# Optimization experiments

Hardware: AMD Instinct MI355X
Metric: run time of the kernel (lower is better)

## Reference

```python
import jax, jax.numpy as jnp
import numpy as np
import math

B, S, STATE, H, D = 4, 2048, 1024, 16, 64
N_ROT = 32  # int(0.5*64), even
ROPE_BASE = 10000.0


def setup_inputs() -> dict:
    key = jax.random.key(0)
    ks = jax.random.split(key, 8)
    q_src = jax.random.normal(ks[0], (B, S, STATE), jnp.float32)
    k_src = jax.random.normal(ks[1], (B, S, STATE), jnp.float32)
    v_src = jax.random.normal(ks[2], (B, S, STATE), jnp.float32)
    # causal position mask: True = masked (torch masked_fill semantics)
    position_mask = jnp.triu(jnp.ones((S, S), jnp.bool_), k=1)
    sd = 0.02
    Wq = jax.random.normal(ks[3], (H * D, STATE), jnp.float32) * sd
    Wk = jax.random.normal(ks[4], (H * D, STATE), jnp.float32) * sd
    Wv = jax.random.normal(ks[5], (H * D, STATE), jnp.float32) * sd
    Wo = jax.random.normal(ks[6], (STATE, H * D), jnp.float32) * sd
    return {"q_src": q_src, "k_src": k_src, "v_src": v_src,
            "position_mask": position_mask,
            "Wq": Wq, "Wk": Wk, "Wv": Wv, "Wo": Wo}


def _rotate_half(x):
    x1, x2 = jnp.split(x, 2, axis=-1)
    return jnp.concatenate([-x2, x1], axis=-1)


def _rope(q, k, offset):
    # q,k: [B,H,S,N_ROT]; positions: k at arange(Sk), q at offset+arange(Sq)
    inv_freq = 1.0 / (ROPE_BASE ** (jnp.arange(0, N_ROT, 2, dtype=jnp.float32) / N_ROT))
    def sincos(pos):
        freqs = pos[:, None] * inv_freq[None, :]          # [S, N_ROT/2]
        emb = jnp.concatenate([freqs, freqs], axis=-1)    # [S, N_ROT]
        return jnp.sin(emb), jnp.cos(emb)
    sk, ck = sincos(jnp.arange(k.shape[-2], dtype=jnp.float32))
    sq, cq = sincos(offset + jnp.arange(q.shape[-2], dtype=jnp.float32))
    q = q * cq + _rotate_half(q) * sq
    k = k * ck + _rotate_half(k) * sk
    return q, k


def reference(q_src, k_src, v_src, position_mask, Wq, Wk, Wv, Wo):
    qk_scale = (1.0 / math.sqrt(D)) ** 0.5  # sqrt of 1/sqrt(D), applied to q and k
    def heads(x):  # [B,S,H*D] -> [B,H,S,D]
        return x.reshape(B, S, H, D).transpose(0, 2, 1, 3)
    q = heads((q_src @ Wq.T) * qk_scale)
    k = heads((k_src @ Wk.T) * qk_scale)
    v = heads(v_src @ Wv.T)
    # inline RoPE on first N_ROT dims (pos_offset = 0, no kv cache)
    rq, rk = _rope(q[..., :N_ROT], k[..., :N_ROT], 0.0)
    q = jnp.concatenate([rq, q[..., N_ROT:]], axis=-1)
    k = jnp.concatenate([rk, k[..., N_ROT:]], axis=-1)
    att = jnp.einsum('bhqd,bhkd->bhqk', q, k)
    att = jnp.where(position_mask[None, None], -jnp.inf, att)
    att = jax.nn.softmax(att, axis=-1)
    out = jnp.einsum('bhqk,bhkd->bhqd', att, v)
    out = out.transpose(0, 2, 1, 3).reshape(B, S, H * D)
    return out @ Wo.T
```

## Files before the change

kernel.cpp:

```cpp
#include <hip/hip_runtime.h>

typedef unsigned short u16;
typedef unsigned int u32;
typedef short short8 __attribute__((ext_vector_type(8)));
typedef float f32x4 __attribute__((ext_vector_type(4)));
typedef float f32x16 __attribute__((ext_vector_type(16)));

#define NB 4
#define NS 2048
#define NSTATE 1024
#define NH 16
#define ND 64
#define NM (NB*NS)

#if __has_builtin(__builtin_amdgcn_exp2f)
#define EXP2(x) __builtin_amdgcn_exp2f(x)
#else
#define EXP2(x) __expf((x) * 0.6931471805599453f)
#endif

__device__ __forceinline__ u16 f2bf(float f){
  union { float fv; unsigned uv; } x; x.fv = f;
  unsigned r = x.uv + 0x7fffu + ((x.uv >> 16) & 1u);
  return (u16)(r >> 16);
}

__device__ __forceinline__ u32 cvtpk(float lo, float hi){
  u32 r;
  asm("v_cvt_pk_bf16_f32 %0, %1, %2" : "=v"(r) : "v"(lo), "v"(hi));
  return r;
}

__device__ __forceinline__ float max3f(float a, float b, float c){
  return fmaxf(fmaxf(a, b), c);
}

__device__ __forceinline__ f32x4 mfma16x16(short8 a, short8 b, f32x4 c){
  return __builtin_amdgcn_mfma_f32_16x16x32_bf16(a, b, c, 0, 0, 0);
}

__device__ __forceinline__ f32x16 mfma32(short8 a, short8 b, f32x16 c){
  return __builtin_amdgcn_mfma_f32_32x32x16_bf16(a, b, c, 0, 0, 0);
}

__device__ __forceinline__ void gld_lds16(const u16* g, u16* l){
  __builtin_amdgcn_global_load_lds((const __attribute__((address_space(1))) void*)g,
                                   (__attribute__((address_space(3))) void*)l, 16, 0, 0);
}

__global__ __launch_bounds__(256)
void cvt_all(const float* __restrict__ q, const float* __restrict__ k, const float* __restrict__ v,
             const float* __restrict__ wq, const float* __restrict__ wk,
             const float* __restrict__ wv, const float* __restrict__ wo,
             u16* oq, u16* ok, u16* ov, u16* owq, u16* owk, u16* owv, u16* owo){
  const int XN4 = (NB*NS*NSTATE)/4;
  const int WN4 = (NSTATE*NSTATE)/4;
  int gid = blockIdx.x * 256 + threadIdx.x;
  const float* src; u16* dst; int idx;
  if (gid < XN4)          { src = q; dst = oq; idx = gid; }
  else if (gid < 2*XN4)   { src = k; dst = ok; idx = gid - XN4; }
  else if (gid < 3*XN4)   { src = v; dst = ov; idx = gid - 2*XN4; }
  else {
    int g = gid - 3*XN4;
    int wsel = g >> 18;
    idx = g & (WN4 - 1);
    src = (wsel==0)?wq:(wsel==1)?wk:(wsel==2)?wv:wo;
    dst = (wsel==0)?owq:(wsel==1)?owk:(wsel==2)?owv:owo;
  }
  float4 val = ((const float4*)src)[idx];
  ushort4 r;
  r.x = f2bf(val.x); r.y = f2bf(val.y); r.z = f2bf(val.z); r.w = f2bf(val.w);
  ((ushort4*)dst)[idx] = r;
}

__global__ __launch_bounds__(256)
void gemm_qkv(const u16* __restrict__ xq, const u16* __restrict__ xk,
              const u16* __restrict__ xv, const u16* __restrict__ Wcat,
              u16* __restrict__ Qh, u16* __restrict__ Kk, u16* __restrict__ Vt){
  __shared__ __align__(16) u16 As[128*64];
  __shared__ __align__(16) u16 Bs[128*64];
  const int gblk = blockIdx.x;
  const int wid = (gblk & 7) * 192 + (gblk >> 3);
  const int bx = wid % 24, by = wid / 24;
  const int sel = bx >> 3;
  const u16* A = (sel==0) ? xq : (sel==1) ? xk : xv;
  const int tid = threadIdx.x;
  const int lane = tid & 63, w = tid >> 6;
  const int wr = w >> 1, wc = w & 1;
  const int l15 = lane & 15, lhi = lane >> 4;
  const int brow = by * 128;
  const int bcol = bx * 128;
  const int K = NSTATE;
  f32x4 acc[4][4] = {};

  int aoffg[4], boffg[4];
  {
    int r0 = tid >> 3;
    int scb = (tid & 7) ^ (r0 & 7);
    #pragma unroll
    for (int it = 0; it < 4; ++it){
      int row = it*32 + r0;
      aoffg[it] = (brow + row)*K + scb*8;
      boffg[it] = (bcol + row)*K + scb*8;
    }
  }
  int afr[4], bfr[4];
  #pragma unroll
  for (int i = 0; i < 4; ++i){
    int rowA = wr*64 + i*16 + l15;
    afr[i] = rowA*64 + ((lhi ^ (rowA & 7))*8);
    int rowB = wc*64 + i*16 + l15;
    bfr[i] = rowB*64 + ((lhi ^ (rowB & 7))*8);
  }

  for (int kt = 0; kt < K; kt += 64){
    #pragma unroll
    for (int it = 0; it < 4; ++it)
      gld_lds16(A + aoffg[it] + kt, As + it*2048 + tid*8);
    #pragma unroll
    for (int it = 0; it < 4; ++it)
      gld_lds16(Wcat + boffg[it] + kt, Bs + it*2048 + tid*8);
    __syncthreads();
    #pragma unroll
    for (int ks = 0; ks < 2; ++ks){
      short8 av[4], bv[4];
      #pragma unroll
      for (int i = 0; i < 4; ++i)
        av[i] = *(const short8*)&As[afr[i] ^ (ks << 5)];
      #pragma unroll
      for (int j = 0; j < 4; ++j)
        bv[j] = *(const short8*)&Bs[bfr[j] ^ (ks << 5)];
      __builtin_amdgcn_s_setprio(1);
      #pragma unroll
      for (int i = 0; i < 4; ++i)
        #pragma unroll
        for (int j = 0; j < 4; ++j)
          acc[i][j] = mfma16x16(av[i], bv[j], acc[i][j]);
      __builtin_amdgcn_s_setprio(0);
    }
    __syncthreads();
  }

  const int col0 = bcol + wc*64;
  if (sel == 2){
    const int head = (col0 & 1023) >> 6;
    #pragma unroll
    for (int i = 0; i < 4; ++i){
      int m0 = brow + wr*64 + i*16 + lhi*4;
      int b = m0 >> 11, s0 = m0 & (NS-1);
      u16* obase = Vt + ((size_t)((b*NH + head)*ND))*NS + s0;
      #pragma unroll
      for (int j = 0; j < 4; ++j){
        int d = j*16 + l15;
        uint2 pk;
        pk.x = cvtpk(acc[i][j][0], acc[i][j][1]);
        pk.y = cvtpk(acc[i][j][2], acc[i][j][3]);
        *(uint2*)(obase + (size_t)d*NS) = pk;
      }
    }
  } else {
    u16* out = sel ? Kk : Qh;
    const float qk_scale = 0.4246609f;
    const int head = (col0 & 1023) >> 6;
    const float invf = EXP2(-0.83048202f * (float)l15);
    #pragma unroll
    for (int i = 0; i < 4; ++i){
      #pragma unroll
      for (int reg = 0; reg < 4; ++reg){
        int m = brow + wr*64 + i*16 + lhi*4 + reg;
        int b = m >> 11, s = m & (NS-1);
        float sn, cs;
        __sincosf((float)s * invf, &sn, &cs);
        float x0 = acc[i][0][reg]*qk_scale;
        float x1 = acc[i][1][reg]*qk_scale;
        u16* orow = out + ((size_t)(b*NH + head)*NS + s)*ND;
        orow[ 0 + l15] = f2bf(x0*cs - x1*sn);
        orow[16 + l15] = f2bf(x1*cs + x0*sn);
        orow[32 + l15] = f2bf(acc[i][2][reg]*qk_scale);
        orow[48 + l15] = f2bf(acc[i][3][reg]*qk_scale);
      }
    }
  }
}

__global__ __launch_bounds__(256)
void gemm_wo(const u16* __restrict__ A, const u16* __restrict__ Bt, float* __restrict__ out){
  __shared__ __align__(16) u16 As[128*64];
  __shared__ __align__(16) u16 Bs[128*64];
  const int gblk = blockIdx.x;
  const int wid = (gblk & 7) * 64 + (gblk >> 3);
  const int bx = wid & 7, by = wid >> 3;
  const int tid = threadIdx.x;
  const int lane = tid & 63, w = tid >> 6;
  const int wr = w >> 1, wc = w & 1;
  const int l15 = lane & 15, lhi = lane >> 4;
  const int brow = by * 128;
  const int bcol = bx * 128;
  const int K = NSTATE;
  f32x4 acc[4][4] = {};

  int aoffg[4], boffg[4];
  {
    int r0 = tid >> 3;
    int scb = (tid & 7) ^ (r0 & 7);
    #pragma unroll
    for (int it = 0; it < 4; ++it){
      int row = it*32 + r0;
      aoffg[it] = (brow + row)*K + scb*8;
      boffg[it] = (bcol + row)*K + scb*8;
    }
  }
  int afr[4], bfr[4];
  #pragma unroll
  for (int i = 0; i < 4; ++i){
    int rowA = wr*64 + i*16 + l15;
    afr[i] = rowA*64 + ((lhi ^ (rowA & 7))*8);
    int rowB = wc*64 + i*16 + l15;
    bfr[i] = rowB*64 + ((lhi ^ (rowB & 7))*8);
  }

  for (int kt = 0; kt < K; kt += 64){
    #pragma unroll
    for (int it = 0; it < 4; ++it)
      gld_lds16(A + aoffg[it] + kt, As + it*2048 + tid*8);
    #pragma unroll
    for (int it = 0; it < 4; ++it)
      gld_lds16(Bt + boffg[it] + kt, Bs + it*2048 + tid*8);
    __syncthreads();
    #pragma unroll
    for (int ks = 0; ks < 2; ++ks){
      short8 av[4], bv[4];
      #pragma unroll
      for (int i = 0; i < 4; ++i)
        av[i] = *(const short8*)&As[afr[i] ^ (ks << 5)];
      #pragma unroll
      for (int j = 0; j < 4; ++j)
        bv[j] = *(const short8*)&Bs[bfr[j] ^ (ks << 5)];
      __builtin_amdgcn_s_setprio(1);
      #pragma unroll
      for (int i = 0; i < 4; ++i)
        #pragma unroll
        for (int j = 0; j < 4; ++j)
          acc[i][j] = mfma16x16(av[i], bv[j], acc[i][j]);
      __builtin_amdgcn_s_setprio(0);
    }
    __syncthreads();
  }
  #pragma unroll
  for (int i = 0; i < 4; ++i)
    #pragma unroll
    for (int reg = 0; reg < 4; ++reg){
      int m = brow + wr*64 + i*16 + lhi*4 + reg;
      float* orow = out + (size_t)m*NSTATE + bcol + wc*64;
      #pragma unroll
      for (int j = 0; j < 4; ++j)
        orow[j*16 + l15] = acc[i][j][reg];
    }
}

__global__ __launch_bounds__(256)
void flash_attn(const u16* __restrict__ Q, const u16* __restrict__ Kh,
                const u16* __restrict__ Vt, u16* __restrict__ O){
  __shared__ __align__(16) u16 Kbuf[2][64*64];
  __shared__ __align__(16) u16 Vbuf[2][64*64];
  const int gblk = blockIdx.x;
  const int xcd = gblk & 7, gr = gblk >> 3;
  const int bh  = xcd*8 + (gr & 7);
  const int c   = gr >> 3;
  const int tid = threadIdx.x;
  const int w = tid >> 6, lane = tid & 63;
  const int l31 = lane & 31, hi = lane >> 5;
  const u16* Qb = Q  + (size_t)bh*NS*ND;
  const u16* Kb = Kh + (size_t)bh*NS*ND;
  const u16* Vb = Vt + (size_t)bh*ND*NS;
  const int b = bh >> 4, h = bh & 15;

  short8 ones;
  #pragma unroll
  for (int i = 0; i < 8; ++i) ones[i] = (short)0x3F80;

  const int r0 = tid >> 3;
  const int scc = (tid & 7) ^ (r0 & 7);
  const u16* ksrc[2]; const u16* vsrc[2];
  #pragma unroll
  for (int i = 0; i < 2; ++i){
    int row = i*32 + r0;
    ksrc[i] = Kb + row*ND + scc*8;
    vsrc[i] = Vb + (size_t)row*NS + scc*8;
  }
  int offs[8];
  #pragma unroll
  for (int a = 0; a < 2; ++a)
    #pragma unroll
    for (int bb = 0; bb < 4; ++bb)
      offs[a*4+bb] = (((a*32 + l31)*128 + bb*32 + hi*16) ^ ((l31 & 7) << 4));

  #pragma unroll 1
  for (int ph = 0; ph < 2; ++ph){
    const int g  = ph ? (15 - c) : c;
    const int qw = g*128 + w*32;
    const int kend_w   = qw + 32;
    const int kend_blk = g*128 + 128;

    short8 qf[4];
    #pragma unroll
    for (int dd = 0; dd < 4; ++dd)
      qf[dd] = *(const short8*)&Qb[(size_t)(qw + l31)*ND + dd*16 + hi*8];

    f32x16 oacc[2] = {};
    f32x16 lacc = {};
    float mrun = 12.0f;

    int cur = 0;
    #pragma unroll
    for (int i = 0; i < 2; ++i){
      gld_lds16(ksrc[i], &Kbuf[0][i*2048 + tid*8]);
      gld_lds16(vsrc[i], &Vbuf[0][i*2048 + tid*8]);
    }
    __syncthreads();

    #pragma unroll 1
    for (int kv0 = 0; kv0 < kend_blk; kv0 += 64){
      if (kv0 + 64 < kend_blk){
        #pragma unroll
        for (int i = 0; i < 2; ++i){
          gld_lds16(ksrc[i] + (kv0 + 64)*ND, &Kbuf[cur^1][i*2048 + tid*8]);
          gld_lds16(vsrc[i] + (kv0 + 64),    &Vbuf[cur^1][i*2048 + tid*8]);
        }
      }
      if (kv0 < kend_w){
        const char* kb = (const char*)&Kbuf[cur][0];
        const char* vb = (const char*)&Vbuf[cur][0];
        short8 kf[8];
        #pragma unroll
        for (int j = 0; j < 8; ++j)
          kf[j] = *(const short8*)(kb + offs[j]);
        f32x16 st0 = {}, st1 = {};
        __builtin_amdgcn_s_setprio(1);
        #pragma unroll
        for (int dd = 0; dd < 4; ++dd) st0 = mfma32(kf[dd],   qf[dd], st0);
        #pragma unroll
        for (int dd = 0; dd < 4; ++dd) st1 = mfma32(kf[4+dd], qf[dd], st1);
        __builtin_amdgcn_s_setprio(0);
        if (kv0 + 63 > qw){
          int q = qw + l31;
          #pragma unroll
          for (int r2 = 0; r2 < 16; ++r2){
            int k0 = kv0 + (r2 & 3) + 8*(r2 >> 2) + 4*hi;
            if (k0      > q) st0[r2] = -3.0e30f;
            if (k0 + 32 > q) st1[r2] = -3.0e30f;
          }
        }
        float t0 = max3f(st0[0],  st0[1],  st0[2]);
        float t1 = max3f(st0[3],  st0[4],  st0[5]);
        float t2 = max3f(st0[6],  st0[7],  st0[8]);
        float t3 = max3f(st0[9],  st0[10], st0[11]);
        float t4 = max3f(st0[12], st0[13], st0[14]);
        float t5 = max3f(st1[0],  st1[1],  st1[2]);
        float t6 = max3f(st1[3],  st1[4],  st1[5]);
        float t7 = max3f(st1[6],  st1[7],  st1[8]);
        float t8 = max3f(st1[9],  st1[10], st1[11]);
        float t9 = max3f(st1[12], st1[13], st1[14]);
        float u0 = max3f(t0, t1, t2);
        float u1 = max3f(t3, t4, st0[15]);
        float u2 = max3f(t5, t6, t7);
        float u3 = max3f(t8, t9, st1[15]);
        float pm = fmaxf(max3f(u0, u1, u2), u3);
        pm = fmaxf(pm, __shfl_xor(pm, 32));
        #pragma unroll
        for (int r2 = 0; r2 < 16; ++r2){
          st0[r2] = EXP2(st0[r2] - mrun);
          st1[r2] = EXP2(st1[r2] - mrun);
        }
        if (__any(pm > mrun)){
          float mn = fmaxf(mrun, pm);
          float a  = EXP2(mrun - mn);
          mrun = mn;
          #pragma unroll
          for (int r2 = 0; r2 < 16; ++r2){
            st0[r2] *= a; st1[r2] *= a;
            oacc[0][r2] *= a; oacc[1][r2] *= a;
            lacc[r2] *= a;
          }
        }
        short8 paf[4];
        #pragma unroll
        for (int sl = 0; sl < 4; ++sl){
          const f32x16& S = (sl < 2) ? st0 : st1;
          const int base = (sl & 1) * 8;
          u32 a0 = cvtpk(S[base+0], S[base+1]);
          u32 b0 = cvtpk(S[base+4], S[base+5]);
          asm("v_permlane32_swap_b32 %0, %1" : "+v"(a0), "+v"(b0));
          u32 a1 = cvtpk(S[base+2], S[base+3]);
          u32 b1 = cvtpk(S[base+6], S[base+7]);
          asm("v_permlane32_swap_b32 %0, %1" : "+v"(a1), "+v"(b1));
          union { u32 u[4]; short8 v; } pk_;
          pk_.u[0] = a0; pk_.u[1] = a1; pk_.u[2] = b0; pk_.u[3] = b1;
          paf[sl] = pk_.v;
        }
        #pragma unroll
        for (int dh = 0; dh < 2; ++dh){
          short8 vv[4];
          #pragma unroll
          for (int sl = 0; sl < 4; ++sl)
            vv[sl] = *(const short8*)(vb + offs[dh*4+sl]);
          __builtin_amdgcn_s_setprio(1);
          #pragma unroll
          for (int sl = 0; sl < 4; ++sl)
            oacc[dh] = mfma32(vv[sl], paf[sl], oacc[dh]);
          __builtin_amdgcn_s_setprio(0);
        }
        __builtin_amdgcn_s_setprio(1);
        #pragma unroll
        for (int sl = 0; sl < 4; ++sl)
          lacc = mfma32(ones, paf[sl], lacc);
        __builtin_amdgcn_s_setprio(0);
      }
      __syncthreads();
      cur ^= 1;
    }

    float inv = 1.0f / lacc[0];
    u16* orow = O + ((size_t)(b*NS + qw + l31))*NSTATE + h*ND;
    #pragma unroll
    for (int dh = 0; dh < 2; ++dh)
      #pragma unroll
      for (int rq = 0; rq < 4; ++rq){
        uint2 pk;
        pk.x = cvtpk(oacc[dh][rq*4+0]*inv, oacc[dh][rq*4+1]*inv);
        pk.y = cvtpk(oacc[dh][rq*4+2]*inv, oacc[dh][rq*4+3]*inv);
        *(uint2*)(orow + dh*32 + rq*8 + hi*4) = pk;
      }
  }
}

extern "C" void kernel_launch(void* const* d_in, const int* in_sizes, int n_in,
                              void* d_out, int out_size, void* d_ws, size_t ws_size,
                              hipStream_t stream){
  const float* q_src = (const float*)d_in[0];
  const float* k_src = (const float*)d_in[1];
  const float* v_src = (const float*)d_in[2];
  const float* Wq = (const float*)d_in[4];
  const float* Wk = (const float*)d_in[5];
  const float* Wv = (const float*)d_in[6];
  const float* Wo = (const float*)d_in[7];

  char* ws = (char*)d_ws;
  const size_t MB = 1u << 20;
  if (ws_size < 104*MB) return;

  u16* xq   = (u16*)(ws +  0*MB);
  u16* xk   = (u16*)(ws + 16*MB);
  u16* xv   = (u16*)(ws + 32*MB);
  u16* wq16 = (u16*)(ws + 48*MB);
  u16* wk16 = (u16*)(ws + 50*MB);
  u16* wv16 = (u16*)(ws + 52*MB);
  u16* wo16 = (u16*)(ws + 54*MB);
  u16* Qh   = (u16*)(ws + 56*MB);
  u16* Kk   = (u16*)(ws + 72*MB);
  u16* Vt   = (u16*)(ws + 88*MB);
  u16* Oat  = xk;

  cvt_all<<<dim3(28672), dim3(256), 0, stream>>>(q_src, k_src, v_src, Wq, Wk, Wv, Wo,
                                                 xq, xk, xv, wq16, wk16, wv16, wo16);
  gemm_qkv<<<dim3(1536), dim3(256), 0, stream>>>(xq, xk, xv, wq16, Qh, Kk, Vt);
  flash_attn<<<dim3(512), dim3(256), 0, stream>>>(Qh, Kk, Vt, Oat);
  gemm_wo<<<dim3(512), dim3(256), 0, stream>>>(Oat, wo16, (float*)d_out);
}
```

Baseline: 189.5 us.

## Add 4-stage async LDS pipelining to GEMMs and flash attention

New measurement: 194.4 us. +2.6%, slower.

```diff
diff --git a/kernel.cpp b/kernel.cpp
--- a/kernel.cpp
+++ b/kernel.cpp
@@ -18,6 +18,8 @@
 #else
 #define EXP2(x) __expf((x) * 0.6931471805599453f)
 #endif
+
+#define SBAR() __builtin_amdgcn_sched_barrier(0)
 
 __device__ __forceinline__ u16 f2bf(float f){
   union { float fv; unsigned uv; } x; x.fv = f;
@@ -73,12 +75,77 @@
   ((ushort4*)dst)[idx] = r;
 }
 
+__device__ __forceinline__ void kloop_bk32(const u16* __restrict__ A, const u16* __restrict__ Bm,
+                                           u16* __restrict__ Ab, u16* __restrict__ Bb,
+                                           int brow, int bcol, int tid, int wr, int wc,
+                                           int l15, int lhi, f32x4 (&acc)[4][4]){
+  const int K = NSTATE;
+  int goA[2], goB[2], ld[2];
+  #pragma unroll
+  for (int i2 = 0; i2 < 2; ++i2){
+    int ch = i2*256 + tid;
+    int row = ch >> 2, cc = ch & 3;
+    int s = (row >> 1) & 3;
+    goA[i2] = (brow + row)*K + (cc ^ s)*8;
+    goB[i2] = (bcol + row)*K + (cc ^ s)*8;
+    ld[i2] = ch*8;
+  }
+  int afr[4], bfr[4];
+  #pragma unroll
+  for (int i = 0; i < 4; ++i){
+    int rA = wr*64 + i*16 + l15;
+    afr[i] = rA*32 + ((lhi ^ ((rA >> 1) & 3))*8);
+    int rB = wc*64 + i*16 + l15;
+    bfr[i] = rB*32 + ((lhi ^ ((rB >> 1) & 3))*8);
+  }
+  auto stage = [&](int t, int b){
+    u16* Ad = Ab + b*4096; u16* Bd = Bb + b*4096;
+    #pragma unroll
+    for (int i2 = 0; i2 < 2; ++i2){
+      gld_lds16(A  + goA[i2] + t*32, Ad + ld[i2]);
+      gld_lds16(Bm + goB[i2] + t*32, Bd + ld[i2]);
+    }
+  };
+  auto compute = [&](int b){
+    const u16* Ax = Ab + b*4096; const u16* Bx = Bb + b*4096;
+    short8 av[4], bv[4];
+    #pragma unroll
+    for (int i = 0; i < 4; ++i) av[i] = *(const short8*)&Ax[afr[i]];
+    #pragma unroll
+    for (int j = 0; j < 4; ++j) bv[j] = *(const short8*)&Bx[bfr[j]];
+    __builtin_amdgcn_s_setprio(1);
+    #pragma unroll
+    for (int i = 0; i < 4; ++i)
+      #pragma unroll
+      for (int j = 0; j < 4; ++j)
+        acc[i][j] = mfma16x16(av[i], bv[j], acc[i][j]);
+    __builtin_amdgcn_s_setprio(0);
+  };
+  stage(0,0); stage(1,1); stage(2,2);
+  #pragma unroll 1
+  for (int t = 0; t < 29; ++t){
+    asm volatile("s_waitcnt vmcnt(8)" ::: "memory");
+    SBAR(); __builtin_amdgcn_s_barrier(); SBAR();
+    stage(t+3, (t+3)&3);
+    compute(t&3);
+  }
+  asm volatile("s_waitcnt vmcnt(8)" ::: "memory");
+  SBAR(); __builtin_amdgcn_s_barrier(); SBAR();
+  compute(1);
+  asm volatile("s_waitcnt vmcnt(4)" ::: "memory");
+  SBAR(); __builtin_amdgcn_s_barrier(); SBAR();
+  compute(2);
+  asm volatile("s_waitcnt vmcnt(0)" ::: "memory");
+  SBAR(); __builtin_amdgcn_s_barrier(); SBAR();
+  compute(3);
+}
+
 __global__ __launch_bounds__(256)
 void gemm_qkv(const u16* __restrict__ xq, const u16* __restrict__ xk,
               const u16* __restrict__ xv, const u16* __restrict__ Wcat,
               u16* __restrict__ Qh, u16* __restrict__ Kk, u16* __restrict__ Vt){
-  __shared__ __align__(16) u16 As[128*64];
-  __shared__ __align__(16) u16 Bs[128*64];
+  __shared__ __align__(16) u16 Ab[4*128*32];
+  __shared__ __align__(16) u16 Bb[4*128*32];
   const int gblk = blockIdx.x;
   const int wid = (gblk & 7) * 192 + (gblk >> 3);
   const int bx = wid % 24, by = wid / 24;
@@ -90,56 +157,9 @@
   const int l15 = lane & 15, lhi = lane >> 4;
   const int brow = by * 128;
   const int bcol = bx * 128;
-  const int K = NSTATE;
   f32x4 acc[4][4] = {};
 
-  int aoffg[4], boffg[4];
-  {
-    int r0 = tid >> 3;
-    int scb = (tid & 7) ^ (r0 & 7);
-    #pragma unroll
-    for (int it = 0; it < 4; ++it){
-      int row = it*32 + r0;
-      aoffg[it] = (brow + row)*K + scb*8;
-      boffg[it] = (bcol + row)*K + scb*8;
-    }
-  }
-  int afr[4], bfr[4];
-  #pragma unroll
-  for (int i = 0; i < 4; ++i){
-    int rowA = wr*64 + i*16 + l15;
-    afr[i] = rowA*64 + ((lhi ^ (rowA & 7))*8);
-    int rowB = wc*64 + i*16 + l15;
-    bfr[i] = rowB*64 + ((lhi ^ (rowB & 7))*8);
-  }
-
-  for (int kt = 0; kt < K; kt += 64){
-    #pragma unroll
-    for (int it = 0; it < 4; ++it)
-      gld_lds16(A + aoffg[it] + kt, As + it*2048 + tid*8);
-    #pragma unroll
-    for (int it = 0; it < 4; ++it)
-      gld_lds16(Wcat + boffg[it] + kt, Bs + it*2048 + tid*8);
-    __syncthreads();
-    #pragma unroll
-    for (int ks = 0; ks < 2; ++ks){
-      short8 av[4], bv[4];
-      #pragma unroll
-      for (int i = 0; i < 4; ++i)
-        av[i] = *(const short8*)&As[afr[i] ^ (ks << 5)];
-      #pragma unroll
-      for (int j = 0; j < 4; ++j)
-        bv[j] = *(const short8*)&Bs[bfr[j] ^ (ks << 5)];
-      __builtin_amdgcn_s_setprio(1);
-      #pragma unroll
-      for (int i = 0; i < 4; ++i)
-        #pragma unroll
-        for (int j = 0; j < 4; ++j)
-          acc[i][j] = mfma16x16(av[i], bv[j], acc[i][j]);
-      __builtin_amdgcn_s_setprio(0);
-    }
-    __syncthreads();
-  }
+  kloop_bk32(A, Wcat, Ab, Bb, brow, bcol, tid, wr, wc, l15, lhi, acc);
 
   const int col0 = bcol + wc*64;
   if (sel == 2){
@@ -185,8 +205,8 @@
 
 __global__ __launch_bounds__(256)
 void gemm_wo(const u16* __restrict__ A, const u16* __restrict__ Bt, float* __restrict__ out){
-  __shared__ __align__(16) u16 As[128*64];
-  __shared__ __align__(16) u16 Bs[128*64];
+  __shared__ __align__(16) u16 Ab[4*128*32];
+  __shared__ __align__(16) u16 Bb[4*128*32];
   const int gblk = blockIdx.x;
   const int wid = (gblk & 7) * 64 + (gblk >> 3);
   const int bx = wid & 7, by = wid >> 3;
@@ -196,56 +216,10 @@
   const int l15 = lane & 15, lhi = lane >> 4;
   const int brow = by * 128;
   const int bcol = bx * 128;
-  const int K = NSTATE;
   f32x4 acc[4][4] = {};
 
-  int aoffg[4], boffg[4];
-  {
-    int r0 = tid >> 3;
-    int scb = (tid & 7) ^ (r0 & 7);
-    #pragma unroll
-    for (int it = 0; it < 4; ++it){
-      int row = it*32 + r0;
-      aoffg[it] = (brow + row)*K + scb*8;
-      boffg[it] = (bcol + row)*K + scb*8;
-    }
-  }
-  int afr[4], bfr[4];
-  #pragma unroll
-  for (int i = 0; i < 4; ++i){
-    int rowA = wr*64 + i*16 + l15;
-    afr[i] = rowA*64 + ((lhi ^ (rowA & 7))*8);
-    int rowB = wc*64 + i*16 + l15;
-    bfr[i] = rowB*64 + ((lhi ^ (rowB & 7))*8);
-  }
-
-  for (int kt = 0; kt < K; kt += 64){
-    #pragma unroll
-    for (int it = 0; it < 4; ++it)
-      gld_lds16(A + aoffg[it] + kt, As + it*2048 + tid*8);
-    #pragma unroll
-    for (int it = 0; it < 4; ++it)
-      gld_lds16(Bt + boffg[it] + kt, Bs + it*2048 + tid*8);
-    __syncthreads();
-    #pragma unroll
-    for (int ks = 0; ks < 2; ++ks){
-      short8 av[4], bv[4];
-      #pragma unroll
-      for (int i = 0; i < 4; ++i)
-        av[i] = *(const short8*)&As[afr[i] ^ (ks << 5)];
-      #pragma unroll
-      for (int j = 0; j < 4; ++j)
-        bv[j] = *(const short8*)&Bs[bfr[j] ^ (ks << 5)];
-      __builtin_amdgcn_s_setprio(1);
-      #pragma unroll
-      for (int i = 0; i < 4; ++i)
-        #pragma unroll
-        for (int j = 0; j < 4; ++j)
-          acc[i][j] = mfma16x16(av[i], bv[j], acc[i][j]);
-      __builtin_amdgcn_s_setprio(0);
-    }
-    __syncthreads();
-  }
+  kloop_bk32(A, Bt, Ab, Bb, brow, bcol, tid, wr, wc, l15, lhi, acc);
+
   #pragma unroll
   for (int i = 0; i < 4; ++i)
     #pragma unroll
@@ -261,8 +235,8 @@
 __global__ __launch_bounds__(256)
 void flash_attn(const u16* __restrict__ Q, const u16* __restrict__ Kh,
                 const u16* __restrict__ Vt, u16* __restrict__ O){
-  __shared__ __align__(16) u16 Kbuf[2][64*64];
-  __shared__ __align__(16) u16 Vbuf[2][64*64];
+  __shared__ __align__(16) u16 Kbuf[4][64*64];
+  __shared__ __align__(16) u16 Vbuf[4][64*64];
   const int gblk = blockIdx.x;
   const int xcd = gblk & 7, gr = gblk >> 3;
   const int bh  = xcd*8 + (gr & 7);
@@ -295,12 +269,21 @@
     for (int bb = 0; bb < 4; ++bb)
       offs[a*4+bb] = (((a*32 + l31)*128 + bb*32 + hi*16) ^ ((l31 & 7) << 4));
 
+  auto stageKV = [&](int t, int bf){
+    u16* kd = &Kbuf[bf][0]; u16* vd = &Vbuf[bf][0];
+    #pragma unroll
+    for (int i = 0; i < 2; ++i){
+      gld_lds16(ksrc[i] + t*64*ND, kd + i*2048 + tid*8);
+      gld_lds16(vsrc[i] + t*64,    vd + i*2048 + tid*8);
+    }
+  };
+
   #pragma unroll 1
   for (int ph = 0; ph < 2; ++ph){
     const int g  = ph ? (15 - c) : c;
     const int qw = g*128 + w*32;
-    const int kend_w   = qw + 32;
-    const int kend_blk = g*128 + 128;
+    const int kend_w = qw + 32;
+    const int nt = (g + 1) * 2;
 
     short8 qf[4];
     #pragma unroll
@@ -311,26 +294,22 @@
     f32x16 lacc = {};
     float mrun = 12.0f;
 
-    int cur = 0;
-    #pragma unroll
-    for (int i = 0; i < 2; ++i){
-      gld_lds16(ksrc[i], &Kbuf[0][i*2048 + tid*8]);
-      gld_lds16(vsrc[i], &Vbuf[0][i*2048 + tid*8]);
-    }
     __syncthreads();
+    #pragma unroll
+    for (int i = 0; i < 3; ++i) if (i < nt) stageKV(i, i);
 
     #pragma unroll 1
-    for (int kv0 = 0; kv0 < kend_blk; kv0 += 64){
-      if (kv0 + 64 < kend_blk){
-        #pragma unroll
-        for (int i = 0; i < 2; ++i){
-          gld_lds16(ksrc[i] + (kv0 + 64)*ND, &Kbuf[cur^1][i*2048 + tid*8]);
-          gld_lds16(vsrc[i] + (kv0 + 64),    &Vbuf[cur^1][i*2048 + tid*8]);
-        }
-      }
+    for (int t = 0; t < nt; ++t){
+      const int rem = nt - t;
+      if (rem > 2)       asm volatile("s_waitcnt vmcnt(8)" ::: "memory");
+      else if (rem == 2) asm volatile("s_waitcnt vmcnt(4)" ::: "memory");
+      else               asm volatile("s_waitcnt vmcnt(0)" ::: "memory");
+      SBAR(); __builtin_amdgcn_s_barrier(); SBAR();
+      if (t + 3 < nt) stageKV(t+3, (t+3)&3);
+      const int kv0 = t*64;
       if (kv0 < kend_w){
-        const char* kb = (const char*)&Kbuf[cur][0];
-        const char* vb = (const char*)&Vbuf[cur][0];
+        const char* kb = (const char*)&Kbuf[t&3][0];
+        const char* vb = (const char*)&Vbuf[t&3][0];
         short8 kf[8];
         #pragma unroll
         for (int j = 0; j < 8; ++j)
@@ -416,8 +395,6 @@
           lacc = mfma32(ones, paf[sl], lacc);
         __builtin_amdgcn_s_setprio(0);
       }
-      __syncthreads();
-      cur ^= 1;
     }
 
     float inv = 1.0f / lacc[0];
```

## Enlarge QKV GEMM tiles to 256x256 with double-buffered LDS prefetch

Applied to the files above, without the earlier changes.

Result: slower. 225.2 us (+18.8%).

```diff
diff --git a/kernel.cpp b/kernel.cpp
--- a/kernel.cpp
+++ b/kernel.cpp
@@ -18,6 +18,8 @@
 #else
 #define EXP2(x) __expf((x) * 0.6931471805599453f)
 #endif
+
+#define SBAR() __builtin_amdgcn_sched_barrier(0)
 
 __device__ __forceinline__ u16 f2bf(float f){
   union { float fv; unsigned uv; } x; x.fv = f;
@@ -73,80 +75,100 @@
   ((ushort4*)dst)[idx] = r;
 }
 
-__global__ __launch_bounds__(256)
+__global__ __launch_bounds__(512)
 void gemm_qkv(const u16* __restrict__ xq, const u16* __restrict__ xk,
               const u16* __restrict__ xv, const u16* __restrict__ Wcat,
               u16* __restrict__ Qh, u16* __restrict__ Kk, u16* __restrict__ Vt){
-  __shared__ __align__(16) u16 As[128*64];
-  __shared__ __align__(16) u16 Bs[128*64];
+  __shared__ __align__(16) u16 Ah[2][2][128*64];
+  __shared__ __align__(16) u16 Bh[2][2][128*64];
   const int gblk = blockIdx.x;
-  const int wid = (gblk & 7) * 192 + (gblk >> 3);
-  const int bx = wid % 24, by = wid / 24;
-  const int sel = bx >> 3;
+  const int wid = (gblk & 7) * 48 + (gblk >> 3);
+  const int bx = wid % 12, by = wid / 12;
+  const int sel = bx >> 2;
   const u16* A = (sel==0) ? xq : (sel==1) ? xk : xv;
   const int tid = threadIdx.x;
   const int lane = tid & 63, w = tid >> 6;
-  const int wr = w >> 1, wc = w & 1;
+  const int wr = w >> 2, wc = w & 3;
   const int l15 = lane & 15, lhi = lane >> 4;
-  const int brow = by * 128;
-  const int bcol = bx * 128;
+  const int brow = by*256, bcol = bx*256;
   const int K = NSTATE;
-  f32x4 acc[4][4] = {};
-
-  int aoffg[4], boffg[4];
-  {
-    int r0 = tid >> 3;
-    int scb = (tid & 7) ^ (r0 & 7);
-    #pragma unroll
-    for (int it = 0; it < 4; ++it){
-      int row = it*32 + r0;
-      aoffg[it] = (brow + row)*K + scb*8;
-      boffg[it] = (bcol + row)*K + scb*8;
-    }
-  }
-  int afr[4], bfr[4];
-  #pragma unroll
-  for (int i = 0; i < 4; ++i){
-    int rowA = wr*64 + i*16 + l15;
-    afr[i] = rowA*64 + ((lhi ^ (rowA & 7))*8);
-    int rowB = wc*64 + i*16 + l15;
-    bfr[i] = rowB*64 + ((lhi ^ (rowB & 7))*8);
-  }
-
-  for (int kt = 0; kt < K; kt += 64){
-    #pragma unroll
-    for (int it = 0; it < 4; ++it)
-      gld_lds16(A + aoffg[it] + kt, As + it*2048 + tid*8);
-    #pragma unroll
-    for (int it = 0; it < 4; ++it)
-      gld_lds16(Wcat + boffg[it] + kt, Bs + it*2048 + tid*8);
-    __syncthreads();
-    #pragma unroll
-    for (int ks = 0; ks < 2; ++ks){
-      short8 av[4], bv[4];
-      #pragma unroll
-      for (int i = 0; i < 4; ++i)
-        av[i] = *(const short8*)&As[afr[i] ^ (ks << 5)];
-      #pragma unroll
-      for (int j = 0; j < 4; ++j)
-        bv[j] = *(const short8*)&Bs[bfr[j] ^ (ks << 5)];
-      __builtin_amdgcn_s_setprio(1);
-      #pragma unroll
-      for (int i = 0; i < 4; ++i)
-        #pragma unroll
-        for (int j = 0; j < 4; ++j)
-          acc[i][j] = mfma16x16(av[i], bv[j], acc[i][j]);
-      __builtin_amdgcn_s_setprio(0);
-    }
-    __syncthreads();
+  f32x4 acc[8][4] = {};
+
+  int srow[2], scb8[2], ldo[2];
+  #pragma unroll
+  for (int i2 = 0; i2 < 2; ++i2){
+    int c = i2*512 + tid;
+    int row = c >> 3, cb = c & 7;
+    srow[i2] = row; scb8[i2] = (cb ^ (row & 7))*8; ldo[i2] = c*8;
+  }
+  int afr[8], bfr[4];
+  #pragma unroll
+  for (int i = 0; i < 8; ++i){
+    int row = i*16 + l15;
+    afr[i] = row*64 + ((lhi ^ (row & 7))*8);
+  }
+  #pragma unroll
+  for (int j = 0; j < 4; ++j){
+    int row = (wc & 1)*64 + j*16 + l15;
+    bfr[j] = row*64 + ((lhi ^ (row & 7))*8);
+  }
+
+  auto stage_half = [&](int T, int hh, int d){
+    int h = hh >> 1;
+    if ((hh & 1) == 0){
+      #pragma unroll
+      for (int i2 = 0; i2 < 2; ++i2)
+        gld_lds16(A + (size_t)(brow + h*128 + srow[i2])*K + T*64 + scb8[i2],
+                  &Ah[d][h][ldo[i2]]);
+    } else {
+      #pragma unroll
+      for (int i2 = 0; i2 < 2; ++i2)
+        gld_lds16(Wcat + (size_t)(bcol + h*128 + srow[i2])*K + T*64 + scb8[i2],
+                  &Bh[d][h][ldo[i2]]);
+    }
+  };
+
+  #pragma unroll
+  for (int hh = 0; hh < 4; ++hh) stage_half(0, hh, 0);
+
+  #pragma unroll 1
+  for (int T = 0; T < 16; ++T){
+    const int cur = T & 1;
+    const u16* Ax = &Ah[cur][wr][0];
+    const u16* Bx = &Bh[cur][wc >> 1][0];
+    asm volatile("s_waitcnt vmcnt(0)" ::: "memory");
+    SBAR(); __builtin_amdgcn_s_barrier(); SBAR();
+    #pragma unroll
+    for (int q = 0; q < 4; ++q){
+      if (T + 1 < 16) stage_half(T+1, q, cur ^ 1);
+      const int i0 = (q >> 1)*4, j0 = (q & 1)*2;
+      #pragma unroll
+      for (int ks = 0; ks < 2; ++ks){
+        short8 av[4], bv[2];
+        #pragma unroll
+        for (int ii = 0; ii < 4; ++ii)
+          av[ii] = *(const short8*)&Ax[afr[i0+ii] ^ (ks << 5)];
+        #pragma unroll
+        for (int jj = 0; jj < 2; ++jj)
+          bv[jj] = *(const short8*)&Bx[bfr[j0+jj] ^ (ks << 5)];
+        __builtin_amdgcn_s_setprio(1);
+        #pragma unroll
+        for (int ii = 0; ii < 4; ++ii)
+          #pragma unroll
+          for (int jj = 0; jj < 2; ++jj)
+            acc[i0+ii][j0+jj] = mfma16x16(av[ii], bv[jj], acc[i0+ii][j0+jj]);
+        __builtin_amdgcn_s_setprio(0);
+      }
+      SBAR(); __builtin_amdgcn_s_barrier(); SBAR();
+    }
   }
 
   const int col0 = bcol + wc*64;
   if (sel == 2){
     const int head = (col0 & 1023) >> 6;
     #pragma unroll
-    for (int i = 0; i < 4; ++i){
-      int m0 = brow + wr*64 + i*16 + lhi*4;
+    for (int i = 0; i < 8; ++i){
+      int m0 = brow + wr*128 + i*16 + lhi*4;
       int b = m0 >> 11, s0 = m0 & (NS-1);
       u16* obase = Vt + ((size_t)((b*NH + head)*ND))*NS + s0;
       #pragma unroll
@@ -164,10 +186,10 @@
     const int head = (col0 & 1023) >> 6;
     const float invf = EXP2(-0.83048202f * (float)l15);
     #pragma unroll
-    for (int i = 0; i < 4; ++i){
+    for (int i = 0; i < 8; ++i){
       #pragma unroll
       for (int reg = 0; reg < 4; ++reg){
-        int m = brow + wr*64 + i*16 + lhi*4 + reg;
+        int m = brow + wr*128 + i*16 + lhi*4 + reg;
         int b = m >> 11, s = m & (NS-1);
         float sn, cs;
         __sincosf((float)s * invf, &sn, &cs);
@@ -463,7 +485,7 @@
 
   cvt_all<<<dim3(28672), dim3(256), 0, stream>>>(q_src, k_src, v_src, Wq, Wk, Wv, Wo,
                                                  xq, xk, xv, wq16, wk16, wv16, wo16);
-  gemm_qkv<<<dim3(1536), dim3(256), 0, stream>>>(xq, xk, xv, wq16, Qh, Kk, Vt);
+  gemm_qkv<<<dim3(384), dim3(512), 0, stream>>>(xq, xk, xv, wq16, Qh, Kk, Vt);
   flash_attn<<<dim3(512), dim3(256), 0, stream>>>(Qh, Kk, Vt, Oat);
   gemm_wo<<<dim3(512), dim3(256), 0, stream>>>(Oat, wo16, (float*)d_out);
 }
```
